# Performance work log

Hardware: AMD Instinct MI355X
Metric: run time of the kernel (lower is better)

## Reference

```python
import jax, jax.numpy as jnp
import numpy as np
from functools import partial

SAMPLE_RATE = 44100
CUTOFF_HZ = 20.0
# one-pole high-pass coefficient: y[i] = x[i] - x[i-1] + alpha * y[i-1]
ALPHA = float(np.exp(-2.0 * np.pi * CUTOFF_HZ / SAMPLE_RATE))


def setup_inputs() -> dict:
    key = jax.random.key(0)
    k1, k2, k3, k4 = jax.random.split(key, 4)
    B, N = 64, 262144
    return {
        "x": jax.random.normal(k1, (B, N), dtype=jnp.float32),
        "drive": jax.random.uniform(k2, (B, 1), dtype=jnp.float32),
        "bias": jax.random.uniform(k3, (B, 1), dtype=jnp.float32),
        "mix": jax.random.uniform(k4, (B, 1), dtype=jnp.float32),
        "type_idx": 0,
    }


def _waveshape(processed, type_idx):
    if type_idx == 0:
        return jnp.tanh(processed)
    elif type_idx == 1:
        return jnp.clip(processed, -1.0, 1.0)
    elif type_idx == 2:
        return jnp.abs(jnp.remainder(processed + 1.0, 4.0) - 2.0) - 1.0
    elif type_idx == 3:
        return jnp.sin(processed * (np.pi / 2))
    else:
        return processed / (1.0 + jnp.abs(processed))


def _high_pass_filter(x):
    # x: [B, N]; sequential first-order IIR over the time axis via lax.scan
    B = x.shape[0]
    zeros = jnp.zeros((B,), dtype=x.dtype)

    def step(carry, xt):
        last_x, last_y = carry
        yt = xt - last_x + ALPHA * last_y
        return (xt, yt), yt

    _, yT = jax.lax.scan(step, (zeros, zeros), x.T)  # yT: [N, B]
    return yT.T


def reference(x, drive, bias, mix, type_idx):
    drive_gain = jnp.power(10.0, drive * 2.4)
    dc_offset = bias * 2.0 - 1.0
    processed = (x + dc_offset) * drive_gain
    distorted = _waveshape(processed, type_idx)
    distorted = _high_pass_filter(distorted)
    return (1.0 - mix) * x + mix * distorted
```

## Files before the change

kernel.cpp:

```cpp
#include <hip/hip_runtime.h>
#include <math.h>

#define TPB 512
#define WAVES (TPB / 64)
#define PER_WAVE 1024
#define CHUNK (WAVES * PER_WAVE)
#define NB 16
#define HALO 2048

typedef float v4f __attribute__((ext_vector_type(4)));

template<int CTRL, int RM, int BM, bool BC>
__device__ __forceinline__ float dppf(float v) {
    return __int_as_float(__builtin_amdgcn_update_dpp(
        0, __float_as_int(v), CTRL, RM, BM, BC));
}

__device__ __forceinline__ float readlane_f(float v, int l) {
    return __int_as_float(__builtin_amdgcn_readlane(__float_as_int(v), l));
}

__device__ __forceinline__ float scan_iir(float v, float mo1, float mo2,
                                          float mo4, float mo8,
                                          float w1, float w2) {
    float b;
    b = dppf<0x111, 0xF, 0xF, true >(v); v = fmaf(mo1, b, v);
    b = dppf<0x112, 0xF, 0xF, true >(v); v = fmaf(mo2, b, v);
    b = dppf<0x114, 0xF, 0xF, true >(v); v = fmaf(mo4, b, v);
    b = dppf<0x118, 0xF, 0xF, true >(v); v = fmaf(mo8, b, v);
    b = dppf<0x142, 0xA, 0xF, false>(v); v = fmaf(w1,  b, v);
    b = dppf<0x143, 0xC, 0xF, false>(v); v = fmaf(w2,  b, v);
    return v;
}

__device__ __forceinline__ float shape(float xs, int ty, float g, float dc,
                                       float c1, float c0) {
    if (ty == 0) {
        float e2 = __builtin_amdgcn_exp2f(fmaf(xs, c1, c0));
        return fmaf(-2.0f, __builtin_amdgcn_rcpf(e2 + 1.0f), 1.0f);
    }
    float p = (xs + dc) * g;
    if (ty == 1) {
        return fminf(fmaxf(p, -1.0f), 1.0f);
    } else if (ty == 2) {
        float r = p + 1.0f;
        float rem = r - 4.0f * floorf(r * 0.25f);
        return fabsf(rem - 2.0f) - 1.0f;
    } else if (ty == 3) {
        return __sinf(p * 1.5707963267948966f);
    } else {
        return p / (1.0f + fabsf(p));
    }
}

__device__ __forceinline__ void load_chunk(v4f xv[4], const float* __restrict__ xr,
                                           int base, int N) {
    #pragma unroll
    for (int k = 0; k < 4; ++k) {
        const int j = base + k * 256;
        if (j + 4 <= N) {
            xv[k] = *reinterpret_cast<const v4f*>(xr + j);
        } else {
            xv[k].x = (j + 0 < N) ? xr[j + 0] : 0.0f;
            xv[k].y = (j + 1 < N) ? xr[j + 1] : 0.0f;
            xv[k].z = (j + 2 < N) ? xr[j + 2] : 0.0f;
            xv[k].w = (j + 3 < N) ? xr[j + 3] : 0.0f;
        }
    }
}

__global__ void __launch_bounds__(TPB, 6)
dist_kernel(const float* __restrict__ x,
            const float* __restrict__ drive,
            const float* __restrict__ bias,
            const float* __restrict__ mix,
            const int* __restrict__ type_idx,
            float* __restrict__ out,
            int N, float alpha, float beta)
{
    const int row  = blockIdx.y;
    const int bx   = blockIdx.x;
    const int tid  = threadIdx.x;
    const int lane = tid & 63;
    const int wv   = tid >> 6;
    const int ty   = *type_idx;

    const int nChunks = (N + CHUNK - 1) / CHUNK;
    const int cpb = (nChunks + NB - 1) / NB;
    const int cFirst = bx * cpb;
    if (cFirst >= nChunks) return;
    const int cLast = min(cFirst + cpb, nChunks);
    const int spanStart = cFirst * CHUNK;

    const float g  = exp2f(drive[row] * 7.972672880099267f);
    const float dc = bias[row] * 2.0f - 1.0f;
    const float mm = mix[row];
    const float om = 1.0f - mm;
    const float c1 = g * 2.8853900817779268f;
    const float c0 = dc * c1;

    const long long rowBase = (long long)row * (long long)N;
    const float* __restrict__ xr = x + rowBase;
    float* __restrict__ outr = out + rowBase;

    const float A2 = alpha * alpha;
    const float A4 = A2 * A2;
    const float A8 = A4 * A4;
    const float A16 = A8 * A8;
    const float A32 = A16 * A16;
    const float A64 = A32 * A32;
    const float A128 = A64 * A64;
    const float A256 = A128 * A128;
    const float A512 = A256 * A256;
    const float A1024 = A512 * A512;

    float p15 = 1.0f;
    {
        float b = A4; const int n = lane & 15;
        #pragma unroll
        for (int i = 0; i < 4; ++i) { if ((n >> i) & 1) p15 *= b; b *= b; }
    }
    const float p31 = (lane & 16) ? p15 * A64  : p15;
    const float apl = (lane & 32) ? p31 * A128 : p31;
    const float w1 = A4 * p15;
    const float w2 = A4 * p31;

    __shared__ float wtot[2][WAVES];
    const int wvOff = wv * PER_WAVE + lane * 4;

    v4f xc[4];
    load_chunk(xc, xr, spanStart + wvOff, N);

    float carry = 0.0f;
    if (bx > 0) {
        const int j = spanStart - HALO + wv * 256 + lane * 4;
        const v4f hx = *reinterpret_cast<const v4f*>(xr + j);
        float r = shape(hx.x, ty, g, dc, c1, c0);
        r = fmaf(alpha, r, shape(hx.y, ty, g, dc, c1, c0));
        r = fmaf(alpha, r, shape(hx.z, ty, g, dc, c1, c0));
        r = fmaf(alpha, r, shape(hx.w, ty, g, dc, c1, c0));
        const float s = scan_iir(r, A4, A8, A16, A32, w1, w2);
        if (lane == 63) wtot[1][wv] = s;
    }
    __syncthreads();
    if (bx > 0) {
        #pragma unroll
        for (int w = 0; w < WAVES; ++w) carry = fmaf(A256, carry, wtot[1][w]);
    }

    int par = 0;
    for (int c = cFirst; c < cLast; ++c, par ^= 1) {
        const int cb = c * CHUNK;
        const bool more = (c + 1 < cLast);
        v4f xn[4];
        if (more) load_chunk(xn, xr, cb + CHUNK + wvOff, N);

        v4f d4[4];
        #pragma unroll
        for (int k = 0; k < 4; ++k) {
            d4[k].x = shape(xc[k].x, ty, g, dc, c1, c0);
            d4[k].y = shape(xc[k].y, ty, g, dc, c1, c0);
            d4[k].z = shape(xc[k].z, ty, g, dc, c1, c0);
            d4[k].w = shape(xc[k].w, ty, g, dc, c1, c0);
        }

        float iv[4];
        #pragma unroll
        for (int k = 0; k < 4; ++k) {
            float acc = d4[k].x;
            acc = fmaf(alpha, acc, d4[k].y);
            acc = fmaf(alpha, acc, d4[k].z);
            acc = fmaf(alpha, acc, d4[k].w);
            iv[k] = scan_iir(acc, A4, A8, A16, A32, w1, w2);
        }

        float Tk[4];
        #pragma unroll
        for (int k = 0; k < 4; ++k) Tk[k] = readlane_f(iv[k], 63);
        const float Twave =
            fmaf(A256, fmaf(A256, fmaf(A256, Tk[0], Tk[1]), Tk[2]), Tk[3]);
        if (lane == 0) wtot[par][wv] = Twave;
        __syncthreads();

        float P = carry;
        for (int w = 0; w < wv; ++w) P = fmaf(A1024, P, wtot[par][w]);
        #pragma unroll
        for (int w = 0; w < WAVES; ++w) carry = fmaf(A1024, carry, wtot[par][w]);

        float S = 0.0f, aK = 1.0f;
        #pragma unroll
        for (int k = 0; k < 4; ++k) {
            const int j = cb + wvOff + k * 256;
            const float Ck = fmaf(aK, P, S);
            const float ex = dppf<0x138, 0xF, 0xF, true>(iv[k]);
            float z = fmaf(apl, Ck, ex);
            v4f ov; float y;
            y = fmaf(-beta, z, d4[k].x); ov.x = fmaf(mm, y, om * xc[k].x); z = fmaf(alpha, z, d4[k].x);
            y = fmaf(-beta, z, d4[k].y); ov.y = fmaf(mm, y, om * xc[k].y); z = fmaf(alpha, z, d4[k].y);
            y = fmaf(-beta, z, d4[k].z); ov.z = fmaf(mm, y, om * xc[k].z); z = fmaf(alpha, z, d4[k].z);
            y = fmaf(-beta, z, d4[k].w); ov.w = fmaf(mm, y, om * xc[k].w);
            if (j + 4 <= N) {
                __builtin_nontemporal_store(ov, reinterpret_cast<v4f*>(outr + j));
            } else {
                if (j + 0 < N) outr[j + 0] = ov.x;
                if (j + 1 < N) outr[j + 1] = ov.y;
                if (j + 2 < N) outr[j + 2] = ov.z;
                if (j + 3 < N) outr[j + 3] = ov.w;
            }
            S = fmaf(A256, S, Tk[k]);
            aK *= A256;
        }

        if (more) {
            #pragma unroll
            for (int k = 0; k < 4; ++k) xc[k] = xn[k];
        }
    }
}

extern "C" void kernel_launch(void* const* d_in, const int* in_sizes, int n_in,
                              void* d_out, int out_size, void* d_ws, size_t ws_size,
                              hipStream_t stream) {
    const float* x     = (const float*)d_in[0];
    const float* drive = (const float*)d_in[1];
    const float* bias  = (const float*)d_in[2];
    const float* mixp  = (const float*)d_in[3];
    const int*   tyi   = (const int*)d_in[4];
    float* out = (float*)d_out;

    const int B = in_sizes[1];
    const int N = in_sizes[0] / B;

    const double alpha_d = exp(-2.0 * M_PI * 20.0 / 44100.0);
    const float alpha = (float)alpha_d;
    const float beta  = (float)(1.0 - alpha_d);

    dim3 grid(NB, B);
    dist_kernel<<<grid, TPB, 0, stream>>>(x, drive, bias, mixp, tyi, out, N, alpha, beta);
}
```

Before: 138.2 us.

## Stage input chunks into double-buffered LDS via global_load_lds, halve per-wave chunk

Input chunks are no longer prefetched into registers. They are copied straight from global memory into a double-buffered shared-memory array with the direct-to-LDS load builtin, and the per-wave chunk is halved from 1024 to 512 elements. The waveshaped values are recomputed from LDS in the output pass instead of being kept in registers. The aim is to cut register pressure and let the next chunk's load overlap the current chunk's scan. In exchange it adds a second block-wide barrier per chunk, repeats the tanh work, and uses 32 KB of LDS per block, which can limit how many blocks fit.

```diff
diff --git a/kernel.cpp b/kernel.cpp
--- a/kernel.cpp
+++ b/kernel.cpp
@@ -3,7 +3,7 @@
 
 #define TPB 512
 #define WAVES (TPB / 64)
-#define PER_WAVE 1024
+#define PER_WAVE 512
 #define CHUNK (WAVES * PER_WAVE)
 #define NB 16
 #define HALO 2048
@@ -18,6 +18,12 @@
 
 __device__ __forceinline__ float readlane_f(float v, int l) {
     return __int_as_float(__builtin_amdgcn_readlane(__float_as_int(v), l));
+}
+
+__device__ __forceinline__ void stage16(const float* __restrict__ g, float* l) {
+    __builtin_amdgcn_global_load_lds(
+        (const __attribute__((address_space(1))) unsigned int*)g,
+        (__attribute__((address_space(3))) unsigned int*)l, 16, 0, 0);
 }
 
 __device__ __forceinline__ float scan_iir(float v, float mo1, float mo2,
@@ -50,22 +56,6 @@
         return __sinf(p * 1.5707963267948966f);
     } else {
         return p / (1.0f + fabsf(p));
-    }
-}
-
-__device__ __forceinline__ void load_chunk(v4f xv[4], const float* __restrict__ xr,
-                                           int base, int N) {
-    #pragma unroll
-    for (int k = 0; k < 4; ++k) {
-        const int j = base + k * 256;
-        if (j + 4 <= N) {
-            xv[k] = *reinterpret_cast<const v4f*>(xr + j);
-        } else {
-            xv[k].x = (j + 0 < N) ? xr[j + 0] : 0.0f;
-            xv[k].y = (j + 1 < N) ? xr[j + 1] : 0.0f;
-            xv[k].z = (j + 2 < N) ? xr[j + 2] : 0.0f;
-            xv[k].w = (j + 3 < N) ? xr[j + 3] : 0.0f;
-        }
     }
 }
 
@@ -92,16 +82,39 @@
     const int cLast = min(cFirst + cpb, nChunks);
     const int spanStart = cFirst * CHUNK;
 
+    const long long rowBase = (long long)row * (long long)N;
+    const float* __restrict__ xr = x + rowBase;
+    float* __restrict__ outr = out + rowBase;
+
+    __shared__ float sbuf[2][CHUNK];
+    __shared__ float wtot[2][WAVES];
+
+    const int ldsBase = wv * PER_WAVE;
+    const int wvOff   = ldsBase + lane * 4;
+
+    if (spanStart + CHUNK <= N) {
+        stage16(xr + spanStart + ldsBase + lane * 4,       &sbuf[0][ldsBase]);
+        stage16(xr + spanStart + ldsBase + 256 + lane * 4, &sbuf[0][ldsBase + 256]);
+    } else {
+        #pragma unroll
+        for (int h = 0; h < 2; ++h) {
+            const int idx = ldsBase + h * 256 + lane * 4;
+            const int j = spanStart + idx;
+            v4f v;
+            v.x = (j + 0 < N) ? xr[j + 0] : 0.0f;
+            v.y = (j + 1 < N) ? xr[j + 1] : 0.0f;
+            v.z = (j + 2 < N) ? xr[j + 2] : 0.0f;
+            v.w = (j + 3 < N) ? xr[j + 3] : 0.0f;
+            *reinterpret_cast<v4f*>(&sbuf[0][idx]) = v;
+        }
+    }
+
     const float g  = exp2f(drive[row] * 7.972672880099267f);
     const float dc = bias[row] * 2.0f - 1.0f;
     const float mm = mix[row];
     const float om = 1.0f - mm;
     const float c1 = g * 2.8853900817779268f;
     const float c0 = dc * c1;
-
-    const long long rowBase = (long long)row * (long long)N;
-    const float* __restrict__ xr = x + rowBase;
-    float* __restrict__ outr = out + rowBase;
 
     const float A2 = alpha * alpha;
     const float A4 = A2 * A2;
@@ -112,7 +125,6 @@
     const float A128 = A64 * A64;
     const float A256 = A128 * A128;
     const float A512 = A256 * A256;
-    const float A1024 = A512 * A512;
 
     float p15 = 1.0f;
     {
@@ -124,12 +136,6 @@
     const float apl = (lane & 32) ? p31 * A128 : p31;
     const float w1 = A4 * p15;
     const float w2 = A4 * p31;
-
-    __shared__ float wtot[2][WAVES];
-    const int wvOff = wv * PER_WAVE + lane * 4;
-
-    v4f xc[4];
-    load_chunk(xc, xr, spanStart + wvOff, N);
 
     float carry = 0.0f;
     if (bx > 0) {
@@ -151,54 +157,64 @@
     int par = 0;
     for (int c = cFirst; c < cLast; ++c, par ^= 1) {
         const int cb = c * CHUNK;
-        const bool more = (c + 1 < cLast);
-        v4f xn[4];
-        if (more) load_chunk(xn, xr, cb + CHUNK + wvOff, N);
-
-        v4f d4[4];
-        #pragma unroll
-        for (int k = 0; k < 4; ++k) {
-            d4[k].x = shape(xc[k].x, ty, g, dc, c1, c0);
-            d4[k].y = shape(xc[k].y, ty, g, dc, c1, c0);
-            d4[k].z = shape(xc[k].z, ty, g, dc, c1, c0);
-            d4[k].w = shape(xc[k].w, ty, g, dc, c1, c0);
-        }
-
-        float iv[4];
-        #pragma unroll
-        for (int k = 0; k < 4; ++k) {
-            float acc = d4[k].x;
-            acc = fmaf(alpha, acc, d4[k].y);
-            acc = fmaf(alpha, acc, d4[k].z);
-            acc = fmaf(alpha, acc, d4[k].w);
+
+        float iv[2];
+        #pragma unroll
+        for (int k = 0; k < 2; ++k) {
+            const v4f xv = *reinterpret_cast<const v4f*>(&sbuf[par][wvOff + k * 256]);
+            float acc = shape(xv.x, ty, g, dc, c1, c0);
+            acc = fmaf(alpha, acc, shape(xv.y, ty, g, dc, c1, c0));
+            acc = fmaf(alpha, acc, shape(xv.z, ty, g, dc, c1, c0));
+            acc = fmaf(alpha, acc, shape(xv.w, ty, g, dc, c1, c0));
             iv[k] = scan_iir(acc, A4, A8, A16, A32, w1, w2);
         }
-
-        float Tk[4];
-        #pragma unroll
-        for (int k = 0; k < 4; ++k) Tk[k] = readlane_f(iv[k], 63);
-        const float Twave =
-            fmaf(A256, fmaf(A256, fmaf(A256, Tk[0], Tk[1]), Tk[2]), Tk[3]);
-        if (lane == 0) wtot[par][wv] = Twave;
+        const float Tk0 = readlane_f(iv[0], 63);
+        const float Tk1 = readlane_f(iv[1], 63);
+        if (lane == 0) wtot[par][wv] = fmaf(A256, Tk0, Tk1);
         __syncthreads();
 
         float P = carry;
-        for (int w = 0; w < wv; ++w) P = fmaf(A1024, P, wtot[par][w]);
-        #pragma unroll
-        for (int w = 0; w < WAVES; ++w) carry = fmaf(A1024, carry, wtot[par][w]);
+        for (int w = 0; w < wv; ++w) P = fmaf(A512, P, wtot[par][w]);
+        #pragma unroll
+        for (int w = 0; w < WAVES; ++w) carry = fmaf(A512, carry, wtot[par][w]);
+
+        if (c + 1 < cLast) {
+            const int nb = cb + CHUNK;
+            if (nb + CHUNK <= N) {
+                stage16(xr + nb + ldsBase + lane * 4,       &sbuf[par ^ 1][ldsBase]);
+                stage16(xr + nb + ldsBase + 256 + lane * 4, &sbuf[par ^ 1][ldsBase + 256]);
+            } else {
+                #pragma unroll
+                for (int h = 0; h < 2; ++h) {
+                    const int idx = ldsBase + h * 256 + lane * 4;
+                    const int j = nb + idx;
+                    v4f v;
+                    v.x = (j + 0 < N) ? xr[j + 0] : 0.0f;
+                    v.y = (j + 1 < N) ? xr[j + 1] : 0.0f;
+                    v.z = (j + 2 < N) ? xr[j + 2] : 0.0f;
+                    v.w = (j + 3 < N) ? xr[j + 3] : 0.0f;
+                    *reinterpret_cast<v4f*>(&sbuf[par ^ 1][idx]) = v;
+                }
+            }
+        }
 
         float S = 0.0f, aK = 1.0f;
         #pragma unroll
-        for (int k = 0; k < 4; ++k) {
+        for (int k = 0; k < 2; ++k) {
             const int j = cb + wvOff + k * 256;
+            const v4f xv = *reinterpret_cast<const v4f*>(&sbuf[par][wvOff + k * 256]);
+            const float d0 = shape(xv.x, ty, g, dc, c1, c0);
+            const float d1 = shape(xv.y, ty, g, dc, c1, c0);
+            const float d2 = shape(xv.z, ty, g, dc, c1, c0);
+            const float d3 = shape(xv.w, ty, g, dc, c1, c0);
             const float Ck = fmaf(aK, P, S);
             const float ex = dppf<0x138, 0xF, 0xF, true>(iv[k]);
             float z = fmaf(apl, Ck, ex);
             v4f ov; float y;
-            y = fmaf(-beta, z, d4[k].x); ov.x = fmaf(mm, y, om * xc[k].x); z = fmaf(alpha, z, d4[k].x);
-            y = fmaf(-beta, z, d4[k].y); ov.y = fmaf(mm, y, om * xc[k].y); z = fmaf(alpha, z, d4[k].y);
-            y = fmaf(-beta, z, d4[k].z); ov.z = fmaf(mm, y, om * xc[k].z); z = fmaf(alpha, z, d4[k].z);
-            y = fmaf(-beta, z, d4[k].w); ov.w = fmaf(mm, y, om * xc[k].w);
+            y = fmaf(-beta, z, d0); ov.x = fmaf(mm, y, om * xv.x); z = fmaf(alpha, z, d0);
+            y = fmaf(-beta, z, d1); ov.y = fmaf(mm, y, om * xv.y); z = fmaf(alpha, z, d1);
+            y = fmaf(-beta, z, d2); ov.z = fmaf(mm, y, om * xv.z); z = fmaf(alpha, z, d2);
+            y = fmaf(-beta, z, d3); ov.w = fmaf(mm, y, om * xv.w);
             if (j + 4 <= N) {
                 __builtin_nontemporal_store(ov, reinterpret_cast<v4f*>(outr + j));
             } else {
@@ -207,14 +223,10 @@
                 if (j + 2 < N) outr[j + 2] = ov.z;
                 if (j + 3 < N) outr[j + 3] = ov.w;
             }
-            S = fmaf(A256, S, Tk[k]);
+            S = fmaf(A256, S, Tk0);
             aK *= A256;
         }
-
-        if (more) {
-            #pragma unroll
-            for (int k = 0; k < 4; ++k) xc[k] = xn[k];
-        }
+        __syncthreads();
     }
 }
 
```

New measurement: 117.8 us. 14.8% less time.
